# Kernel tuning notes

Measured on AMD Instinct MI355X. Metric: run time of the kernel, lower is better.

The kernel has to match this reference:

```python
import jax, jax.numpy as jnp
import numpy as np

N, T, P = 8192, 2048, 24  # batch of series, time steps, seasonal period


def setup_inputs() -> dict:
    key = jax.random.key(0)
    k1, k2, k3, k4, k5, k6, k7 = jax.random.split(key, 7)
    return {
        "temp": jax.random.normal(k1, (N, T), dtype=jnp.float32),
        "alpha": jax.random.uniform(k2, (1,), dtype=jnp.float32),
        "beta": jax.random.uniform(k3, (1,), dtype=jnp.float32),
        "gamma": jax.random.uniform(k4, (1,), dtype=jnp.float32),
        "L0": jax.random.normal(k5, (N,), dtype=jnp.float32),
        "b0": jax.random.normal(k6, (N,), dtype=jnp.float32),
        "S0": jax.random.normal(k7, (N, P), dtype=jnp.float32),
        "seasonp": P,
    }


def reference(temp, alpha, beta, gamma, L0, b0, S0, seasonp):
    # Holt-Winters exponential smoothing recurrence (add trend), batched over N series.
    a, bt, g = alpha[0], beta[0], gamma[0]
    Tn = temp.shape[1]
    phases = jnp.arange(1, Tn, dtype=jnp.int32) % seasonp  # i % seasonp
    xs = temp[:, 1:].T  # [T-1, N]

    def step(carry, inp):
        L, b, buf = carry          # L,b: [N]; buf: [N, P] rolling seasonal buffer
        x, ph = inp
        s_read = buf[:, ph]        # S[i % seasonp] (most recent value at this phase)
        Ln = a * (x - s_read) + (1.0 - a) * (L + b)
        bn = bt * (Ln - L) + (1.0 - bt) * b
        sn = g * (x - Ln) + (1.0 - g) * s_read
        buf = buf.at[:, ph].set(sn)
        return (Ln, bn, buf), (Ln, bn, sn)

    (_, _, _), (Ls, bs, Ss) = jax.lax.scan(step, (L0, b0, S0), (xs, phases))
    L = jnp.concatenate([L0[:, None], Ls.T], axis=1)   # [N, T]
    b = jnp.concatenate([b0[:, None], bs.T], axis=1)   # [N, T]
    S = jnp.concatenate([S0[:, 0:1], Ss.T], axis=1)    # [N, T]
    return (L + b) * S
```

## Files before the change

### kernel.cpp

```cpp
#include <hip/hip_runtime.h>


#define STR2 100

__global__ __launch_bounds__(64, 1) void hw_kernel(
    const float* __restrict__ temp,
    const float* __restrict__ alpha,
    const float* __restrict__ beta,
    const float* __restrict__ gamma,
    const float* __restrict__ L0,
    const float* __restrict__ b0,
    const float* __restrict__ S0,
    float* __restrict__ out,
    int N, int T)
{
    __shared__ float ot[64 * STR2];

    const int lane = threadIdx.x;
    const int row0 = blockIdx.x * 64;
    const int row  = row0 + lane;

    const float a_  = alpha[0];
    const float bt  = beta[0];
    const float g_  = gamma[0];
    const float oma = 1.0f - a_;
    const float omb = 1.0f - bt;
    const float opb = 1.0f + bt;
    const float omg = 1.0f - g_;

    const float* xrow = temp + (size_t)row * T;

    float x0[24], x1[24], x2[24], x3[24], x4[24], x5[24], buf[24];
    float L, c;
    float og[4] = {0.f, 0.f, 0.f, 0.f};

#define LOADG(B, T0, J) \
    if ((T0) + 4*(J) + 4 <= T) { \
        const float4 v = *reinterpret_cast<const float4*>(xrow + (T0) + 4*(J)); \
        B[4*(J)+0]=v.x; B[4*(J)+1]=v.y; B[4*(J)+2]=v.z; B[4*(J)+3]=v.w; }
#define LOADX(B, T0) { LOADG(B,(T0),0) LOADG(B,(T0),1) LOADG(B,(T0),2) \
                       LOADG(B,(T0),3) LOADG(B,(T0),4) LOADG(B,(T0),5) }

    LOADX(x0, 0)   LOADX(x1, 24)  LOADX(x2, 48)
    LOADX(x3, 72)  LOADX(x4, 96)  LOADX(x5, 120)
    {
        const float* s0r = S0 + (size_t)row * 24;
        #pragma unroll
        for (int p = 0; p < 6; ++p) {
            const float4 v = *reinterpret_cast<const float4*>(s0r + 4*p);
            buf[4*p+0]=v.x; buf[4*p+1]=v.y; buf[4*p+2]=v.z; buf[4*p+3]=v.w;
        }
        L = L0[row];
        c = L + b0[row];
    }

#define STEPQ(K, B, Q) { \
    const float x  = B[(K)]; \
    const float s  = buf[(K)]; \
    const float Ln = fmaf(oma, c, a_ * (x - s)); \
    const float t1 = fmaf(omb, c, -L); \
    const float cn = fmaf(opb, Ln, t1); \
    const float sn = fmaf(g_, x - Ln, omg * s); \
    buf[(K)] = sn; \
    og[(K)&3] = cn * sn; \
    L = Ln; c = cn; \
    if (((K)&3) == 3) \
        *reinterpret_cast<float4*>(&ot[lane*STR2 + 24*(Q) + ((K)-3)]) = \
            make_float4(og[0], og[1], og[2], og[3]); }

#define CHUNK(B, Q) { \
    STEPQ(0,B,Q)  STEPQ(1,B,Q)  STEPQ(2,B,Q)  STEPQ(3,B,Q)  \
    STEPQ(4,B,Q)  STEPQ(5,B,Q)  STEPQ(6,B,Q)  STEPQ(7,B,Q)  \
    STEPQ(8,B,Q)  STEPQ(9,B,Q)  STEPQ(10,B,Q) STEPQ(11,B,Q) \
    STEPQ(12,B,Q) STEPQ(13,B,Q) STEPQ(14,B,Q) STEPQ(15,B,Q) \
    STEPQ(16,B,Q) STEPQ(17,B,Q) STEPQ(18,B,Q) STEPQ(19,B,Q) \
    STEPQ(20,B,Q) STEPQ(21,B,Q) STEPQ(22,B,Q) STEPQ(23,B,Q) }

#define TSTEPQ(K, B, Q, TF) if ((TF) + 24*(Q) + (K) < T) STEPQ(K, B, Q)
#define TCHUNK(B, Q, TF) { \
    TSTEPQ(0,B,Q,TF)  TSTEPQ(1,B,Q,TF)  TSTEPQ(2,B,Q,TF)  TSTEPQ(3,B,Q,TF)  \
    TSTEPQ(4,B,Q,TF)  TSTEPQ(5,B,Q,TF)  TSTEPQ(6,B,Q,TF)  TSTEPQ(7,B,Q,TF)  \
    TSTEPQ(8,B,Q,TF)  TSTEPQ(9,B,Q,TF)  TSTEPQ(10,B,Q,TF) TSTEPQ(11,B,Q,TF) \
    TSTEPQ(12,B,Q,TF) TSTEPQ(13,B,Q,TF) TSTEPQ(14,B,Q,TF) TSTEPQ(15,B,Q,TF) \
    TSTEPQ(16,B,Q,TF) TSTEPQ(17,B,Q,TF) TSTEPQ(18,B,Q,TF) TSTEPQ(19,B,Q,TF) \
    TSTEPQ(20,B,Q,TF) TSTEPQ(21,B,Q,TF) TSTEPQ(22,B,Q,TF) TSTEPQ(23,B,Q,TF) }

#define WINDOW(P0, P1, P2, P3, WT) { \
    CHUNK(P0, 0) LOADX(P0, (WT) + 144)      \
    CHUNK(P1, 1) LOADX(P1, (WT) + 144 + 24) \
    CHUNK(P2, 2) LOADX(P2, (WT) + 144 + 48) \
    CHUNK(P3, 3) LOADX(P3, (WT) + 144 + 72) }

    const int dr2 = lane >> 3;
    const int dc  = lane & 7;
#define DRAIN(W0) { \
    _Pragma("unroll") for (int rg = 0; rg < 8; ++rg) { \
      _Pragma("unroll") for (int j = 0; j < 3; ++j) { \
        const float4 v = *reinterpret_cast<const float4*>( \
            &ot[(8*rg + dr2)*STR2 + 32*j + 4*dc]); \
        *reinterpret_cast<float4*>( \
            out + (size_t)(row0 + 8*rg + dr2)*T + (W0) + 32*j + 4*dc) = v; \
    } } }

    og[0] = c * buf[0];
    STEPQ(1,x0,0)  STEPQ(2,x0,0)  STEPQ(3,x0,0)
    STEPQ(4,x0,0)  STEPQ(5,x0,0)  STEPQ(6,x0,0)  STEPQ(7,x0,0)
    STEPQ(8,x0,0)  STEPQ(9,x0,0)  STEPQ(10,x0,0) STEPQ(11,x0,0)
    STEPQ(12,x0,0) STEPQ(13,x0,0) STEPQ(14,x0,0) STEPQ(15,x0,0)
    STEPQ(16,x0,0) STEPQ(17,x0,0) STEPQ(18,x0,0) STEPQ(19,x0,0)
    STEPQ(20,x0,0) STEPQ(21,x0,0) STEPQ(22,x0,0) STEPQ(23,x0,0)
    LOADX(x0, 144)
    CHUNK(x1, 1) LOADX(x1, 168)
    CHUNK(x2, 2) LOADX(x2, 192)
    CHUNK(x3, 3) LOADX(x3, 216)
    DRAIN(0)

    for (int g = 0; g < 6; ++g) {
        const int tg = 96 * (3*g + 1);
        WINDOW(x4, x5, x0, x1, tg)        DRAIN(tg)
        WINDOW(x2, x3, x4, x5, tg + 96)   DRAIN(tg + 96)
        WINDOW(x0, x1, x2, x3, tg + 192)  DRAIN(tg + 192)
    }

    WINDOW(x4, x5, x0, x1, 1824)  DRAIN(1824)
    WINDOW(x2, x3, x4, x5, 1920)  DRAIN(1920)

    TCHUNK(x0, 0, 2016)
    TCHUNK(x1, 1, 2016)
    {
        #pragma unroll
        for (int rg = 0; rg < 8; ++rg) {
            const float4 v = *reinterpret_cast<const float4*>(
                &ot[(8*rg + dr2)*STR2 + 4*dc]);
            *reinterpret_cast<float4*>(
                out + (size_t)(row0 + 8*rg + dr2)*T + 2016 + 4*dc) = v;
        }
    }

#undef STEPQ
#undef CHUNK
#undef TSTEPQ
#undef TCHUNK
#undef WINDOW
#undef DRAIN
#undef LOADG
#undef LOADX
}

extern "C" void kernel_launch(void* const* d_in, const int* in_sizes, int n_in,
                              void* d_out, int out_size, void* d_ws, size_t ws_size,
                              hipStream_t stream) {
    const float* temp  = (const float*)d_in[0];
    const float* alpha = (const float*)d_in[1];
    const float* beta  = (const float*)d_in[2];
    const float* gamma = (const float*)d_in[3];
    const float* L0    = (const float*)d_in[4];
    const float* b0    = (const float*)d_in[5];
    const float* S0    = (const float*)d_in[6];
    float* out = (float*)d_out;

    const int N = in_sizes[4];
    const int T = in_sizes[0] / N;

    const int grid = (N + 63) / 64;
    hw_kernel<<<grid, 64, 0, stream>>>(
        temp, alpha, beta, gamma, L0, b0, S0, out, N, T);
}
```

Measured before the change: 52.32 us.

## Stage input tiles in LDS via async global_load_lds with swizzled coalesced reads

Replaces the per-lane strided row loads into six register buffers with a double-buffered LDS staging scheme. Each 96-step tile for 64 rows is copied with global_load_lds, so consecutive lanes read contiguous 16-byte chunks, and an XOR swizzle avoids bank conflicts on readback. The per-step math is also simplified by reusing x-s in the seasonal update. This frees a large number of VGPRs and coalesces the global reads, at the cost of LDS traffic, manual vmcnt waits and tail handling that assumes T is a multiple of 32 past the last full window.

```diff
diff --git a/kernel.cpp b/kernel.cpp
--- a/kernel.cpp
+++ b/kernel.cpp
@@ -1,7 +1,5 @@
 #include <hip/hip_runtime.h>
 
-
-#define STR2 100
 
 __global__ __launch_bounds__(64, 1) void hw_kernel(
     const float* __restrict__ temp,
@@ -14,11 +12,34 @@
     float* __restrict__ out,
     int N, int T)
 {
-    __shared__ float ot[64 * STR2];
+    __shared__ float xlds[2 * 6144];
+    __shared__ float ot[64 * 100];
 
     const int lane = threadIdx.x;
     const int row0 = blockIdx.x * 64;
     const int row  = row0 + lane;
+    const int ln8  = lane >> 3;
+    const int l7   = lane & 7;
+    const int xcol = 4 * (l7 ^ ln8);
+    const int EX   = 16 * l7;
+
+    const float* lanebase = temp + (size_t)(row0 + ln8) * T + xcol;
+    const char*  xrb = (const char*)xlds + ln8 * 3072 + l7 * 128;
+
+#define GLL_TILE(TB, PARF, NK) { \
+    _Pragma("unroll") for (int j = 0; j < 8; ++j) { \
+      _Pragma("unroll") for (int k = 0; k < (NK); ++k) { \
+        __builtin_amdgcn_global_load_lds( \
+          (const __attribute__((address_space(1))) void*)(lanebase + (size_t)(8*j)*T + (TB) + 32*k), \
+          (__attribute__((address_space(3))) void*)(&xlds[(PARF) + (j*3 + k) * 256]), \
+          16, 0, 0); \
+    } } }
+
+#define XRD(XV, Q, PARB) { XV = *reinterpret_cast<const float4*>( \
+        xrb + (PARB) + 1024*((Q) >> 3) + ((16*((Q) & 7)) ^ EX)); }
+
+    GLL_TILE(0,   0,    3)
+    GLL_TILE(96,  6144, 3)
 
     const float a_  = alpha[0];
     const float bt  = beta[0];
@@ -26,23 +47,8 @@
     const float oma = 1.0f - a_;
     const float omb = 1.0f - bt;
     const float opb = 1.0f + bt;
-    const float omg = 1.0f - g_;
 
-    const float* xrow = temp + (size_t)row * T;
-
-    float x0[24], x1[24], x2[24], x3[24], x4[24], x5[24], buf[24];
-    float L, c;
-    float og[4] = {0.f, 0.f, 0.f, 0.f};
-
-#define LOADG(B, T0, J) \
-    if ((T0) + 4*(J) + 4 <= T) { \
-        const float4 v = *reinterpret_cast<const float4*>(xrow + (T0) + 4*(J)); \
-        B[4*(J)+0]=v.x; B[4*(J)+1]=v.y; B[4*(J)+2]=v.z; B[4*(J)+3]=v.w; }
-#define LOADX(B, T0) { LOADG(B,(T0),0) LOADG(B,(T0),1) LOADG(B,(T0),2) \
-                       LOADG(B,(T0),3) LOADG(B,(T0),4) LOADG(B,(T0),5) }
-
-    LOADX(x0, 0)   LOADX(x1, 24)  LOADX(x2, 48)
-    LOADX(x3, 72)  LOADX(x4, 96)  LOADX(x5, 120)
+    float buf[24];
     {
         const float* s0r = S0 + (size_t)row * 24;
         #pragma unroll
@@ -50,101 +56,106 @@
             const float4 v = *reinterpret_cast<const float4*>(s0r + 4*p);
             buf[4*p+0]=v.x; buf[4*p+1]=v.y; buf[4*p+2]=v.z; buf[4*p+3]=v.w;
         }
-        L = L0[row];
-        c = L + b0[row];
     }
+    float L = L0[row];
+    float c = L + b0[row];
+    float og[4] = {0.f, 0.f, 0.f, 0.f};
 
-#define STEPQ(K, B, Q) { \
-    const float x  = B[(K)]; \
-    const float s  = buf[(K)]; \
-    const float Ln = fmaf(oma, c, a_ * (x - s)); \
+#define STEP(Q, E, XE) { \
+    const float x  = (XE); \
+    const float s  = buf[(4*(Q)+(E)) % 24]; \
+    const float t_ = x - s; \
+    const float Ln = fmaf(oma, c, a_ * t_); \
     const float t1 = fmaf(omb, c, -L); \
     const float cn = fmaf(opb, Ln, t1); \
-    const float sn = fmaf(g_, x - Ln, omg * s); \
-    buf[(K)] = sn; \
-    og[(K)&3] = cn * sn; \
-    L = Ln; c = cn; \
-    if (((K)&3) == 3) \
-        *reinterpret_cast<float4*>(&ot[lane*STR2 + 24*(Q) + ((K)-3)]) = \
-            make_float4(og[0], og[1], og[2], og[3]); }
+    const float sn = fmaf(g_, t_ - Ln, s); \
+    buf[(4*(Q)+(E)) % 24] = sn; \
+    og[(E)] = cn * sn; \
+    L = Ln; c = cn; }
 
-#define CHUNK(B, Q) { \
-    STEPQ(0,B,Q)  STEPQ(1,B,Q)  STEPQ(2,B,Q)  STEPQ(3,B,Q)  \
-    STEPQ(4,B,Q)  STEPQ(5,B,Q)  STEPQ(6,B,Q)  STEPQ(7,B,Q)  \
-    STEPQ(8,B,Q)  STEPQ(9,B,Q)  STEPQ(10,B,Q) STEPQ(11,B,Q) \
-    STEPQ(12,B,Q) STEPQ(13,B,Q) STEPQ(14,B,Q) STEPQ(15,B,Q) \
-    STEPQ(16,B,Q) STEPQ(17,B,Q) STEPQ(18,B,Q) STEPQ(19,B,Q) \
-    STEPQ(20,B,Q) STEPQ(21,B,Q) STEPQ(22,B,Q) STEPQ(23,B,Q) }
+#define GROUP(Q, XV) { \
+    STEP(Q,0,(XV).x) STEP(Q,1,(XV).y) STEP(Q,2,(XV).z) STEP(Q,3,(XV).w) \
+    *reinterpret_cast<float4*>((char*)ot + lane*400 + 16*(Q)) = \
+        make_float4(og[0], og[1], og[2], og[3]); }
 
-#define TSTEPQ(K, B, Q, TF) if ((TF) + 24*(Q) + (K) < T) STEPQ(K, B, Q)
-#define TCHUNK(B, Q, TF) { \
-    TSTEPQ(0,B,Q,TF)  TSTEPQ(1,B,Q,TF)  TSTEPQ(2,B,Q,TF)  TSTEPQ(3,B,Q,TF)  \
-    TSTEPQ(4,B,Q,TF)  TSTEPQ(5,B,Q,TF)  TSTEPQ(6,B,Q,TF)  TSTEPQ(7,B,Q,TF)  \
-    TSTEPQ(8,B,Q,TF)  TSTEPQ(9,B,Q,TF)  TSTEPQ(10,B,Q,TF) TSTEPQ(11,B,Q,TF) \
-    TSTEPQ(12,B,Q,TF) TSTEPQ(13,B,Q,TF) TSTEPQ(14,B,Q,TF) TSTEPQ(15,B,Q,TF) \
-    TSTEPQ(16,B,Q,TF) TSTEPQ(17,B,Q,TF) TSTEPQ(18,B,Q,TF) TSTEPQ(19,B,Q,TF) \
-    TSTEPQ(20,B,Q,TF) TSTEPQ(21,B,Q,TF) TSTEPQ(22,B,Q,TF) TSTEPQ(23,B,Q,TF) }
-
-#define WINDOW(P0, P1, P2, P3, WT) { \
-    CHUNK(P0, 0) LOADX(P0, (WT) + 144)      \
-    CHUNK(P1, 1) LOADX(P1, (WT) + 144 + 24) \
-    CHUNK(P2, 2) LOADX(P2, (WT) + 144 + 48) \
-    CHUNK(P3, 3) LOADX(P3, (WT) + 144 + 72) }
+#define WINGRP_REST(PARB) \
+    GROUP(1,xb)  XRD(xb,4,PARB)  GROUP(2,xc)  XRD(xc,5,PARB)  \
+    GROUP(3,xa)  XRD(xa,6,PARB)  GROUP(4,xb)  XRD(xb,7,PARB)  \
+    GROUP(5,xc)  XRD(xc,8,PARB)  GROUP(6,xa)  XRD(xa,9,PARB)  \
+    GROUP(7,xb)  XRD(xb,10,PARB) GROUP(8,xc)  XRD(xc,11,PARB) \
+    GROUP(9,xa)  XRD(xa,12,PARB) GROUP(10,xb) XRD(xb,13,PARB) \
+    GROUP(11,xc) XRD(xc,14,PARB) GROUP(12,xa) XRD(xa,15,PARB) \
+    GROUP(13,xb) XRD(xb,16,PARB) GROUP(14,xc) XRD(xc,17,PARB) \
+    GROUP(15,xa) XRD(xa,18,PARB) GROUP(16,xb) XRD(xb,19,PARB) \
+    GROUP(17,xc) XRD(xc,20,PARB) GROUP(18,xa) XRD(xa,21,PARB) \
+    GROUP(19,xb) XRD(xb,22,PARB) GROUP(20,xc) XRD(xc,23,PARB) \
+    GROUP(21,xa) GROUP(22,xb)    GROUP(23,xc)
 
     const int dr2 = lane >> 3;
     const int dc  = lane & 7;
 #define DRAIN(W0) { \
     _Pragma("unroll") for (int rg = 0; rg < 8; ++rg) { \
-      _Pragma("unroll") for (int j = 0; j < 3; ++j) { \
+      _Pragma("unroll") for (int j2 = 0; j2 < 3; ++j2) { \
         const float4 v = *reinterpret_cast<const float4*>( \
-            &ot[(8*rg + dr2)*STR2 + 32*j + 4*dc]); \
+            (const char*)ot + (8*rg + dr2)*400 + 128*j2 + 16*dc); \
         *reinterpret_cast<float4*>( \
-            out + (size_t)(row0 + 8*rg + dr2)*T + (W0) + 32*j + 4*dc) = v; \
+            out + (size_t)(row0 + 8*rg + dr2)*T + (W0) + 32*j2 + 4*dc) = v; \
     } } }
 
-    og[0] = c * buf[0];
-    STEPQ(1,x0,0)  STEPQ(2,x0,0)  STEPQ(3,x0,0)
-    STEPQ(4,x0,0)  STEPQ(5,x0,0)  STEPQ(6,x0,0)  STEPQ(7,x0,0)
-    STEPQ(8,x0,0)  STEPQ(9,x0,0)  STEPQ(10,x0,0) STEPQ(11,x0,0)
-    STEPQ(12,x0,0) STEPQ(13,x0,0) STEPQ(14,x0,0) STEPQ(15,x0,0)
-    STEPQ(16,x0,0) STEPQ(17,x0,0) STEPQ(18,x0,0) STEPQ(19,x0,0)
-    STEPQ(20,x0,0) STEPQ(21,x0,0) STEPQ(22,x0,0) STEPQ(23,x0,0)
-    LOADX(x0, 144)
-    CHUNK(x1, 1) LOADX(x1, 168)
-    CHUNK(x2, 2) LOADX(x2, 192)
-    CHUNK(x3, 3) LOADX(x3, 216)
+    const int NW = T / 96;
+    float4 xa, xb, xc;
+
+    asm volatile("s_waitcnt vmcnt(24)" ::: "memory");
+    XRD(xa,0,0) XRD(xb,1,0) XRD(xc,2,0)
+    {
+        og[0] = c * buf[0];
+        STEP(0,1,xa.y) STEP(0,2,xa.z) STEP(0,3,xa.w)
+        *reinterpret_cast<float4*>((char*)ot + lane*400) =
+            make_float4(og[0], og[1], og[2], og[3]);
+        XRD(xa,3,0)
+    }
+    WINGRP_REST(0)
     DRAIN(0)
 
-    for (int g = 0; g < 6; ++g) {
-        const int tg = 96 * (3*g + 1);
-        WINDOW(x4, x5, x0, x1, tg)        DRAIN(tg)
-        WINDOW(x2, x3, x4, x5, tg + 96)   DRAIN(tg + 96)
-        WINDOW(x0, x1, x2, x3, tg + 192)  DRAIN(tg + 192)
+    for (int m = 1; m < NW; ++m) {
+        asm volatile("s_waitcnt vmcnt(24)" ::: "memory");
+        const int parb  = (m & 1) * 24576;
+        const int parfN = ((m + 1) & 1) * 6144;
+        const int tbN   = 96 * (m + 1);
+        if (m + 1 < NW) { GLL_TILE(tbN, parfN, 3) }
+        else            { GLL_TILE(tbN, parfN, 1) }
+        XRD(xa,0,parb) XRD(xb,1,parb) XRD(xc,2,parb)
+        GROUP(0,xa) XRD(xa,3,parb)
+        WINGRP_REST(parb)
+        DRAIN(96 * m)
     }
 
-    WINDOW(x4, x5, x0, x1, 1824)  DRAIN(1824)
-    WINDOW(x2, x3, x4, x5, 1920)  DRAIN(1920)
-
-    TCHUNK(x0, 0, 2016)
-    TCHUNK(x1, 1, 2016)
     {
+        asm volatile("s_waitcnt vmcnt(24)" ::: "memory");
+        const int parb = (NW & 1) * 24576;
+        XRD(xa,0,parb) XRD(xb,1,parb) XRD(xc,2,parb)
+        GROUP(0,xa) XRD(xa,3,parb)
+        GROUP(1,xb) XRD(xb,4,parb)
+        GROUP(2,xc) XRD(xc,5,parb)
+        GROUP(3,xa) XRD(xa,6,parb)
+        GROUP(4,xb) XRD(xb,7,parb)
+        GROUP(5,xc) GROUP(6,xa) GROUP(7,xb)
+        const int tf = 96 * NW;
         #pragma unroll
         for (int rg = 0; rg < 8; ++rg) {
             const float4 v = *reinterpret_cast<const float4*>(
-                &ot[(8*rg + dr2)*STR2 + 4*dc]);
+                (const char*)ot + (8*rg + dr2)*400 + 16*dc);
             *reinterpret_cast<float4*>(
-                out + (size_t)(row0 + 8*rg + dr2)*T + 2016 + 4*dc) = v;
+                out + (size_t)(row0 + 8*rg + dr2)*T + tf + 4*dc) = v;
         }
     }
 
-#undef STEPQ
-#undef CHUNK
-#undef TSTEPQ
-#undef TCHUNK
-#undef WINDOW
+#undef STEP
+#undef GROUP
+#undef WINGRP_REST
 #undef DRAIN
-#undef LOADG
-#undef LOADX
+#undef XRD
+#undef GLL_TILE
 }
 
 extern "C" void kernel_launch(void* const* d_in, const int* in_sizes, int n_in,
```

After: 77.59 us. 1.48x slower.

## Halve rows per block to spread the recurrence across all CUs

Applied to the files above, without the earlier changes.

Each 64-thread block now advances only 32 series, with lanes 32-63 idle during the recurrence but still helping drain the shared-memory staging tile. The grid doubles so that more compute units each run one latency-bound recurrence wave, and per-wave drain and store traffic is halved. The register prefetch ring shrinks from six chunks to four, with a plain rolled window loop instead of the manually rotated buffers. The seasonal update is also refactored to reuse x-s and drop one multiply. The trade-offs are half-empty waves during the serial chain and a shallower prefetch distance that may expose load latency.

```diff
diff --git a/kernel.cpp b/kernel.cpp
--- a/kernel.cpp
+++ b/kernel.cpp
@@ -1,6 +1,7 @@
 #include <hip/hip_runtime.h>
 
 
+#define RPB 32
 #define STR2 100
 
 __global__ __launch_bounds__(64, 1) void hw_kernel(
@@ -14,11 +15,12 @@
     float* __restrict__ out,
     int N, int T)
 {
-    __shared__ float ot[64 * STR2];
+    __shared__ float ot[RPB * STR2];
 
     const int lane = threadIdx.x;
-    const int row0 = blockIdx.x * 64;
+    const int row0 = blockIdx.x * RPB;
     const int row  = row0 + lane;
+    const bool comp = (lane < RPB);
 
     const float a_  = alpha[0];
     const float bt  = beta[0];
@@ -26,12 +28,11 @@
     const float oma = 1.0f - a_;
     const float omb = 1.0f - bt;
     const float opb = 1.0f + bt;
-    const float omg = 1.0f - g_;
 
     const float* xrow = temp + (size_t)row * T;
 
-    float x0[24], x1[24], x2[24], x3[24], x4[24], x5[24], buf[24];
-    float L, c;
+    float x0[24], x1[24], x2[24], x3[24], buf[24];
+    float L = 0.f, c = 0.f;
     float og[4] = {0.f, 0.f, 0.f, 0.f};
 
 #define LOADG(B, T0, J) \
@@ -41,9 +42,8 @@
 #define LOADX(B, T0) { LOADG(B,(T0),0) LOADG(B,(T0),1) LOADG(B,(T0),2) \
                        LOADG(B,(T0),3) LOADG(B,(T0),4) LOADG(B,(T0),5) }
 
-    LOADX(x0, 0)   LOADX(x1, 24)  LOADX(x2, 48)
-    LOADX(x3, 72)  LOADX(x4, 96)  LOADX(x5, 120)
-    {
+    if (comp) {
+        LOADX(x0, 0)  LOADX(x1, 24)  LOADX(x2, 48)  LOADX(x3, 72)
         const float* s0r = S0 + (size_t)row * 24;
         #pragma unroll
         for (int p = 0; p < 6; ++p) {
@@ -57,10 +57,11 @@
 #define STEPQ(K, B, Q) { \
     const float x  = B[(K)]; \
     const float s  = buf[(K)]; \
-    const float Ln = fmaf(oma, c, a_ * (x - s)); \
+    const float t_ = x - s; \
+    const float Ln = fmaf(oma, c, a_ * t_); \
     const float t1 = fmaf(omb, c, -L); \
     const float cn = fmaf(opb, Ln, t1); \
-    const float sn = fmaf(g_, x - Ln, omg * s); \
+    const float sn = fmaf(g_, t_ - Ln, s); \
     buf[(K)] = sn; \
     og[(K)&3] = cn * sn; \
     L = Ln; c = cn; \
@@ -85,55 +86,61 @@
     TSTEPQ(16,B,Q,TF) TSTEPQ(17,B,Q,TF) TSTEPQ(18,B,Q,TF) TSTEPQ(19,B,Q,TF) \
     TSTEPQ(20,B,Q,TF) TSTEPQ(21,B,Q,TF) TSTEPQ(22,B,Q,TF) TSTEPQ(23,B,Q,TF) }
 
-#define WINDOW(P0, P1, P2, P3, WT) { \
-    CHUNK(P0, 0) LOADX(P0, (WT) + 144)      \
-    CHUNK(P1, 1) LOADX(P1, (WT) + 144 + 24) \
-    CHUNK(P2, 2) LOADX(P2, (WT) + 144 + 48) \
-    CHUNK(P3, 3) LOADX(P3, (WT) + 144 + 72) }
-
     const int dr2 = lane >> 3;
     const int dc  = lane & 7;
 #define DRAIN(W0) { \
-    _Pragma("unroll") for (int rg = 0; rg < 8; ++rg) { \
-      _Pragma("unroll") for (int j = 0; j < 3; ++j) { \
+    _Pragma("unroll") for (int rg = 0; rg < 4; ++rg) { \
+      _Pragma("unroll") for (int j2 = 0; j2 < 3; ++j2) { \
         const float4 v = *reinterpret_cast<const float4*>( \
-            &ot[(8*rg + dr2)*STR2 + 32*j + 4*dc]); \
+            &ot[(8*rg + dr2)*STR2 + 32*j2 + 4*dc]); \
         *reinterpret_cast<float4*>( \
-            out + (size_t)(row0 + 8*rg + dr2)*T + (W0) + 32*j + 4*dc) = v; \
+            out + (size_t)(row0 + 8*rg + dr2)*T + (W0) + 32*j2 + 4*dc) = v; \
     } } }
 
-    og[0] = c * buf[0];
-    STEPQ(1,x0,0)  STEPQ(2,x0,0)  STEPQ(3,x0,0)
-    STEPQ(4,x0,0)  STEPQ(5,x0,0)  STEPQ(6,x0,0)  STEPQ(7,x0,0)
-    STEPQ(8,x0,0)  STEPQ(9,x0,0)  STEPQ(10,x0,0) STEPQ(11,x0,0)
-    STEPQ(12,x0,0) STEPQ(13,x0,0) STEPQ(14,x0,0) STEPQ(15,x0,0)
-    STEPQ(16,x0,0) STEPQ(17,x0,0) STEPQ(18,x0,0) STEPQ(19,x0,0)
-    STEPQ(20,x0,0) STEPQ(21,x0,0) STEPQ(22,x0,0) STEPQ(23,x0,0)
-    LOADX(x0, 144)
-    CHUNK(x1, 1) LOADX(x1, 168)
-    CHUNK(x2, 2) LOADX(x2, 192)
-    CHUNK(x3, 3) LOADX(x3, 216)
+    const int NW = T / 96;
+    const int tf = NW * 96;
+    const int Lv = T - tf;
+
+    if (comp) {
+        og[0] = c * buf[0];
+        STEPQ(1,x0,0)  STEPQ(2,x0,0)  STEPQ(3,x0,0)
+        STEPQ(4,x0,0)  STEPQ(5,x0,0)  STEPQ(6,x0,0)  STEPQ(7,x0,0)
+        STEPQ(8,x0,0)  STEPQ(9,x0,0)  STEPQ(10,x0,0) STEPQ(11,x0,0)
+        STEPQ(12,x0,0) STEPQ(13,x0,0) STEPQ(14,x0,0) STEPQ(15,x0,0)
+        STEPQ(16,x0,0) STEPQ(17,x0,0) STEPQ(18,x0,0) STEPQ(19,x0,0)
+        STEPQ(20,x0,0) STEPQ(21,x0,0) STEPQ(22,x0,0) STEPQ(23,x0,0)
+        LOADX(x0, 96)
+        CHUNK(x1, 1) LOADX(x1, 120)
+        CHUNK(x2, 2) LOADX(x2, 144)
+        CHUNK(x3, 3) LOADX(x3, 168)
+    }
     DRAIN(0)
 
-    for (int g = 0; g < 6; ++g) {
-        const int tg = 96 * (3*g + 1);
-        WINDOW(x4, x5, x0, x1, tg)        DRAIN(tg)
-        WINDOW(x2, x3, x4, x5, tg + 96)   DRAIN(tg + 96)
-        WINDOW(x0, x1, x2, x3, tg + 192)  DRAIN(tg + 192)
+    for (int m = 1; m < NW; ++m) {
+        const int wt = 96 * m;
+        if (comp) {
+            CHUNK(x0, 0) LOADX(x0, wt + 96)
+            CHUNK(x1, 1) LOADX(x1, wt + 120)
+            CHUNK(x2, 2) LOADX(x2, wt + 144)
+            CHUNK(x3, 3) LOADX(x3, wt + 168)
+        }
+        DRAIN(wt)
     }
 
-    WINDOW(x4, x5, x0, x1, 1824)  DRAIN(1824)
-    WINDOW(x2, x3, x4, x5, 1920)  DRAIN(1920)
-
-    TCHUNK(x0, 0, 2016)
-    TCHUNK(x1, 1, 2016)
-    {
+    if (Lv > 0) {
+        if (comp) {
+            TCHUNK(x0, 0, tf)
+            TCHUNK(x1, 1, tf)
+        }
         #pragma unroll
-        for (int rg = 0; rg < 8; ++rg) {
-            const float4 v = *reinterpret_cast<const float4*>(
-                &ot[(8*rg + dr2)*STR2 + 4*dc]);
-            *reinterpret_cast<float4*>(
-                out + (size_t)(row0 + 8*rg + dr2)*T + 2016 + 4*dc) = v;
+        for (int rg = 0; rg < 4; ++rg) {
+            const int base = 4*dc;
+            if (base + 4 <= Lv) {
+                const float4 v = *reinterpret_cast<const float4*>(
+                    &ot[(8*rg + dr2)*STR2 + base]);
+                *reinterpret_cast<float4*>(
+                    out + (size_t)(row0 + 8*rg + dr2)*T + tf + base) = v;
+            }
         }
     }
 
@@ -141,7 +148,6 @@
 #undef CHUNK
 #undef TSTEPQ
 #undef TCHUNK
-#undef WINDOW
 #undef DRAIN
 #undef LOADG
 #undef LOADX
@@ -162,7 +168,7 @@
     const int N = in_sizes[4];
     const int T = in_sizes[0] / N;
 
-    const int grid = (N + 63) / 64;
+    const int grid = (N + RPB - 1) / RPB;
     hw_kernel<<<grid, 64, 0, stream>>>(
         temp, alpha, beta, gamma, L0, b0, S0, out, N, T);
 }
```

Result: slower. 68.62 us (+31.1%).
